# Optimization experiments

Hardware: AMD Instinct MI355X
Metric: run time of the kernel (lower is better)

Reference implementation:

```python
import jax, jax.numpy as jnp
import numpy as np

DIM = 768
HEADS = 12
HIDDEN = 4 * DIM
B, N = 8, 1024
EPS = 1e-5


def setup_inputs() -> dict:
    key = jax.random.key(0)
    ks = jax.random.split(key, 8)
    s = 0.02
    return {
        "x": jax.random.normal(ks[0], (B, N, DIM), dtype=jnp.float32),
        "ln1_g": jnp.ones((DIM,), jnp.float32),
        "ln1_b": jnp.zeros((DIM,), jnp.float32),
        "qkv_w": jax.random.normal(ks[1], (3 * DIM, DIM), jnp.float32) * s,
        "proj_w": jax.random.normal(ks[2], (DIM, DIM), jnp.float32) * s,
        "proj_b": jnp.zeros((DIM,), jnp.float32),
        "ln2_g": jnp.ones((DIM,), jnp.float32),
        "ln2_b": jnp.zeros((DIM,), jnp.float32),
        "fc1_w": jax.random.normal(ks[3], (HIDDEN, DIM), jnp.float32) * s,
        "fc1_b": jnp.zeros((HIDDEN,), jnp.float32),
        "fc2_w": jax.random.normal(ks[4], (DIM, HIDDEN), jnp.float32) * s,
        "fc2_b": jnp.zeros((DIM,), jnp.float32),
    }


def _layernorm(x, g, b):
    mu = jnp.mean(x, axis=-1, keepdims=True)
    var = jnp.mean(jnp.square(x - mu), axis=-1, keepdims=True)
    return (x - mu) * jax.lax.rsqrt(var + EPS) * g + b


def reference(x, ln1_g, ln1_b, qkv_w, proj_w, proj_b, ln2_g, ln2_b, fc1_w, fc1_b, fc2_w, fc2_b):
    Bn, Nn, C = x.shape
    H = HEADS
    D = C // H
    scale = D ** -0.5

    # --- attention branch ---
    h = _layernorm(x, ln1_g, ln1_b)
    qkv = h @ qkv_w.T                      # [B,N,3C] (qkv_bias=False)
    qkv = qkv.reshape(Bn, Nn, 3, H, D)
    q = qkv[:, :, 0].transpose(0, 2, 1, 3)  # [B,H,N,D]
    k = qkv[:, :, 1].transpose(0, 2, 1, 3)
    v = qkv[:, :, 2].transpose(0, 2, 1, 3)
    attn = jnp.einsum('bhnd,bhmd->bhnm', q, k) * scale  # [B,H,N,N]
    attn = jax.nn.softmax(attn, axis=-1)
    ctx = jnp.einsum('bhnm,bhmd->bhnd', attn, v)         # [B,H,N,D]
    ctx = ctx.transpose(0, 2, 1, 3).reshape(Bn, Nn, C)
    x = x + ctx @ proj_w.T + proj_b

    # --- MLP branch ---
    h = _layernorm(x, ln2_g, ln2_b)
    h = jax.nn.gelu(h @ fc1_w.T + fc1_b, approximate=False)
    return x + h @ fc2_w.T + fc2_b
```

## Files before the change

kernel.cpp:

```cpp
#include <hip/hip_runtime.h>
#include <cstdint>

typedef __attribute__((ext_vector_type(8))) short short8;
typedef __attribute__((ext_vector_type(4))) float f32x4;
typedef unsigned short u16t;

__device__ __forceinline__ u16t f2bf(float f) {
  uint32_t u = __float_as_uint(f);
  u += 0x7fffu + ((u >> 16) & 1u);
  return (u16t)(u >> 16);
}

__device__ __forceinline__ uint32_t cvtpk(float lo, float hi) {
  uint32_t r;
  asm("v_cvt_pk_bf16_f32 %0, %1, %2" : "=v"(r) : "v"(lo), "v"(hi));
  return r;
}

__device__ __forceinline__ void gload_lds16(const void* g, void* l) {
  __builtin_amdgcn_global_load_lds(
      (const __attribute__((address_space(1))) void*)g,
      (__attribute__((address_space(3))) void*)l, 16, 0, 0);
}

__global__ __launch_bounds__(256) void cvt_bf16_kernel(const float* __restrict__ in,
                                                       u16t* __restrict__ out, int n8) {
  int i = blockIdx.x * 256 + threadIdx.x;
  if (i >= n8) return;
  const float4* p = (const float4*)in + (size_t)i * 2;
  float4 a = p[0], b = p[1];
  union { short8 v; u16t e[8]; } r;
  r.e[0] = f2bf(a.x); r.e[1] = f2bf(a.y); r.e[2] = f2bf(a.z); r.e[3] = f2bf(a.w);
  r.e[4] = f2bf(b.x); r.e[5] = f2bf(b.y); r.e[6] = f2bf(b.z); r.e[7] = f2bf(b.w);
  *((short8*)out + i) = r.v;
}

__global__ __launch_bounds__(256) void ln_kernel(const float* __restrict__ x,
                                                 const float* __restrict__ g,
                                                 const float* __restrict__ b,
                                                 u16t* __restrict__ out) {
  int row = blockIdx.x, tid = threadIdx.x;
  int wave = tid >> 6, lane = tid & 63;
  const float* xr = x + (size_t)row * 768;
  float v0 = xr[tid], v1 = xr[tid + 256], v2 = xr[tid + 512];
  float s = v0 + v1 + v2;
  float q = v0 * v0 + v1 * v1 + v2 * v2;
#pragma unroll
  for (int m = 32; m >= 1; m >>= 1) {
    s += __shfl_xor(s, m, 64);
    q += __shfl_xor(q, m, 64);
  }
  __shared__ float red[8];
  if (lane == 0) { red[wave] = s; red[4 + wave] = q; }
  __syncthreads();
  s = red[0] + red[1] + red[2] + red[3];
  q = red[4] + red[5] + red[6] + red[7];
  float mu = s * (1.0f / 768.0f);
  float var = q * (1.0f / 768.0f) - mu * mu;
  float rs = rsqrtf(var + 1e-5f);
  u16t* orow = out + (size_t)row * 768;
  orow[tid]       = f2bf((v0 - mu) * rs * g[tid]       + b[tid]);
  orow[tid + 256] = f2bf((v1 - mu) * rs * g[tid + 256] + b[tid + 256]);
  orow[tid + 512] = f2bf((v2 - mu) * rs * g[tid + 512] + b[tid + 512]);
}

template <int EPI, int BM, int MINB>
__global__ __launch_bounds__(256, MINB) void gemm_bt(const u16t* __restrict__ A,
                                                     const u16t* __restrict__ W,
                                                     void* __restrict__ Cout,
                                                     const float* __restrict__ bias,
                                                     const float* __restrict__ res,
                                                     int M, int N, int K) {
  __shared__ __align__(16) u16t As[BM * 64];
  __shared__ __align__(16) u16t Bs[128 * 64];
  constexpr int MF = BM / 32;
  int tid = threadIdx.x;
  int wave = tid >> 6, lane = tid & 63;
  int wr = wave >> 1, wc = wave & 1;
  int bm = blockIdx.y * BM;
  int bn = blockIdx.x * 128;
  f32x4 acc[MF][4] = {};

  int lr = lane >> 3;
  int lc = lane & 7;
  int srcslot = lc ^ lr;
  const u16t* Abase = A + (size_t)(bm + lr) * K + srcslot * 8;
  const u16t* Wbase = W + (size_t)(bn + lr) * K + srcslot * 8;

  for (int kt = 0; kt < K; kt += 64) {
    __syncthreads();
#pragma unroll
    for (int i = 0; i < BM / 32; i++) {
      int chunk = wave * (BM / 32) + i;
      gload_lds16(Abase + (size_t)(chunk * 8) * K + kt, (void*)(As + chunk * 512));
    }
#pragma unroll
    for (int i = 0; i < 4; i++) {
      int chunk = wave * 4 + i;
      gload_lds16(Wbase + (size_t)(chunk * 8) * K + kt, (void*)(Bs + chunk * 512));
    }
    __syncthreads();

    short8 af[MF][2], bfr[4][2];
#pragma unroll
    for (int m = 0; m < MF; m++) {
      int row = wr * (BM / 2) + m * 16 + (lane & 15);
#pragma unroll
      for (int s = 0; s < 2; s++) {
        int slot = s * 4 + (lane >> 4);
        af[m][s] = *(const short8*)(As + row * 64 + ((slot ^ (row & 7)) * 8));
      }
    }
#pragma unroll
    for (int n = 0; n < 4; n++) {
      int row = wc * 64 + n * 16 + (lane & 15);
#pragma unroll
      for (int s = 0; s < 2; s++) {
        int slot = s * 4 + (lane >> 4);
        bfr[n][s] = *(const short8*)(Bs + row * 64 + ((slot ^ (row & 7)) * 8));
      }
    }
    __builtin_amdgcn_s_setprio(1);
#pragma unroll
    for (int m = 0; m < MF; m++)
#pragma unroll
      for (int n = 0; n < 4; n++) {
        acc[m][n] = __builtin_amdgcn_mfma_f32_16x16x32_bf16(af[m][0], bfr[n][0], acc[m][n], 0, 0, 0);
        acc[m][n] = __builtin_amdgcn_mfma_f32_16x16x32_bf16(af[m][1], bfr[n][1], acc[m][n], 0, 0, 0);
      }
    __builtin_amdgcn_s_setprio(0);
  }

#pragma unroll
  for (int m = 0; m < MF; m++) {
#pragma unroll
    for (int n = 0; n < 4; n++) {
      int r0 = bm + wr * (BM / 2) + m * 16 + (lane >> 4) * 4;
      int c = bn + wc * 64 + n * 16 + (lane & 15);
#pragma unroll
      for (int i = 0; i < 4; i++) {
        int r = r0 + i;
        float v = acc[m][n][i];
        if constexpr (EPI == 0) {
          ((u16t*)Cout)[(size_t)r * N + c] = f2bf(v);
        } else if constexpr (EPI == 1) {
          ((float*)Cout)[(size_t)r * N + c] = v + bias[c] + res[(size_t)r * N + c];
        } else {
          v += bias[c];
          float gl = 0.5f * v * (1.0f + erff(v * 0.70710678118f));
          ((u16t*)Cout)[(size_t)r * N + c] = f2bf(gl);
        }
      }
    }
  }
}

__global__ __launch_bounds__(256) void vtrans_kernel(const u16t* __restrict__ qkv,
                                                     u16t* __restrict__ vt) {
  __shared__ u16t T[64][66];
  int h = blockIdx.x % 12, bb = blockIdx.x / 12, kt = blockIdx.y * 64;
  int t = threadIdx.x;
  int r = t >> 2, dc = t & 3;
  const u16t* src = qkv + (size_t)(bb * 1024 + kt + r) * 2304 + 1536 + h * 64 + dc * 16;
  union { uint4 u[2]; u16t e[16]; uint32_t w[8]; } buf;
  buf.u[0] = *(const uint4*)src;
  buf.u[1] = *(const uint4*)(src + 8);
#pragma unroll
  for (int j = 0; j < 8; j++)
    *(uint32_t*)&T[r][dc * 16 + 2 * j] = buf.w[j];
  __syncthreads();
  int d = t >> 2, kc = t & 3;
  union { uint4 u[2]; u16t e[16]; } o;
#pragma unroll
  for (int j = 0; j < 16; j++) o.e[j] = T[kc * 16 + j][d];
  u16t* dst = vt + ((size_t)blockIdx.x * 64 + d) * 1024 + kt + kc * 16;
  *(uint4*)dst = o.u[0];
  *(uint4*)(dst + 8) = o.u[1];
}

__global__ __launch_bounds__(256, 3) void attn_kernel(const u16t* __restrict__ qkv,
                                                      const u16t* __restrict__ vt,
                                                      u16t* __restrict__ ctx) {
  __shared__ __align__(16) u16t Ks[2][64 * 64];
  __shared__ __align__(16) u16t Vs[2][64 * 64];
  __shared__ __align__(16) u16t Plds[4][32 * 72];
  int tid = threadIdx.x;
  int wave = tid >> 6, lane = tid & 63;
  int q = lane & 15, g = lane >> 4;

  int bid = blockIdx.x;
  int xcd = bid & 7, j = bid >> 3;
  int head = xcd + 8 * (j >> 3);
  int qt = (j & 7) * 128 + wave * 32;
  int b = head / 12, h = head % 12;

  const u16t* base = qkv + (size_t)b * 1024 * 2304 + h * 64;
  const u16t* kbase = base + 768;
  const u16t* vtb = vt + (size_t)head * 64 * 1024;

  short8 qf[2][2];
#pragma unroll
  for (int hf = 0; hf < 2; hf++)
#pragma unroll
    for (int hh = 0; hh < 2; hh++)
      qf[hf][hh] = *(const short8*)(base + (size_t)(qt + hf * 16 + q) * 2304 + hh * 32 + g * 8);

  int lr = lane >> 3, lc = lane & 7;
  const u16t* ksrc = kbase + (size_t)lr * 2304 + (size_t)((lc ^ lr) * 8);
  const u16t* vsrc = vtb + (size_t)lr * 1024 + (size_t)((lc ^ lr) * 8);
  int c0 = wave * 2, c1 = wave * 2 + 1;

  auto stage = [&](int kt, int buf) {
    gload_lds16(ksrc + (size_t)(kt + c0 * 8) * 2304, (void*)(Ks[buf] + c0 * 512));
    gload_lds16(ksrc + (size_t)(kt + c1 * 8) * 2304, (void*)(Ks[buf] + c1 * 512));
    gload_lds16(vsrc + (size_t)(c0 * 8) * 1024 + kt, (void*)(Vs[buf] + c0 * 512));
    gload_lds16(vsrc + (size_t)(c1 * 8) * 1024 + kt, (void*)(Vs[buf] + c1 * 512));
  };

  float mA = -1e30f, mB = -1e30f, lA = 0.f, lB = 0.f;
  f32x4 oA[4] = {}, oB[4] = {};
  u16t* Pw = Plds[wave];

  stage(0, 0);
  __syncthreads();

  for (int t = 0; t < 16; ++t) {
    int buf = t & 1;
    if (t < 15) stage((t + 1) * 64, buf ^ 1);

    const u16t* Kb = Ks[buf];
    const u16t* Vb = Vs[buf];

    f32x4 sA[4] = {}, sB[4] = {};
    __builtin_amdgcn_s_setprio(1);
#pragma unroll
    for (int n = 0; n < 4; n++) {
      int row = n * 16 + q;
      short8 k0 = *(const short8*)(Kb + row * 64 + ((g ^ (q & 7)) * 8));
      short8 k1 = *(const short8*)(Kb + row * 64 + (((4 + g) ^ (q & 7)) * 8));
      sA[n] = __builtin_amdgcn_mfma_f32_16x16x32_bf16(k0, qf[0][0], sA[n], 0, 0, 0);
      sA[n] = __builtin_amdgcn_mfma_f32_16x16x32_bf16(k1, qf[0][1], sA[n], 0, 0, 0);
      sB[n] = __builtin_amdgcn_mfma_f32_16x16x32_bf16(k0, qf[1][0], sB[n], 0, 0, 0);
      sB[n] = __builtin_amdgcn_mfma_f32_16x16x32_bf16(k1, qf[1][1], sB[n], 0, 0, 0);
    }
    __builtin_amdgcn_s_setprio(0);

    float alphaA, alphaB;
    {
      float t0 = fmaxf(fmaxf(sA[0][0], sA[0][1]), fmaxf(sA[0][2], sA[0][3]));
      float t1 = fmaxf(fmaxf(sA[1][0], sA[1][1]), fmaxf(sA[1][2], sA[1][3]));
      float t2 = fmaxf(fmaxf(sA[2][0], sA[2][1]), fmaxf(sA[2][2], sA[2][3]));
      float t3 = fmaxf(fmaxf(sA[3][0], sA[3][1]), fmaxf(sA[3][2], sA[3][3]));
      float tm = fmaxf(fmaxf(t0, t1), fmaxf(t2, t3));
      tm = fmaxf(tm, __shfl_xor(tm, 16, 64));
      tm = fmaxf(tm, __shfl_xor(tm, 32, 64));
      float mnew = fmaxf(mA, tm);
      alphaA = __expf((mA - mnew) * 0.125f);
      mA = mnew;
#pragma unroll
      for (int n = 0; n < 4; n++)
#pragma unroll
        for (int i = 0; i < 4; i++) sA[n][i] = __expf((sA[n][i] - mnew) * 0.125f);
      float r0 = (sA[0][0] + sA[0][1]) + (sA[0][2] + sA[0][3]);
      float r1 = (sA[1][0] + sA[1][1]) + (sA[1][2] + sA[1][3]);
      float r2 = (sA[2][0] + sA[2][1]) + (sA[2][2] + sA[2][3]);
      float r3 = (sA[3][0] + sA[3][1]) + (sA[3][2] + sA[3][3]);
      float rs = (r0 + r1) + (r2 + r3);
      rs += __shfl_xor(rs, 16, 64);
      rs += __shfl_xor(rs, 32, 64);
      lA = lA * alphaA + rs;
#pragma unroll
      for (int n = 0; n < 4; n++) {
        uint32_t w0 = cvtpk(sA[n][0], sA[n][1]);
        uint32_t w1 = cvtpk(sA[n][2], sA[n][3]);
        *(uint2*)(Pw + q * 72 + n * 16 + g * 4) = make_uint2(w0, w1);
      }
    }
    {
      float t0 = fmaxf(fmaxf(sB[0][0], sB[0][1]), fmaxf(sB[0][2], sB[0][3]));
      float t1 = fmaxf(fmaxf(sB[1][0], sB[1][1]), fmaxf(sB[1][2], sB[1][3]));
      float t2 = fmaxf(fmaxf(sB[2][0], sB[2][1]), fmaxf(sB[2][2], sB[2][3]));
      float t3 = fmaxf(fmaxf(sB[3][0], sB[3][1]), fmaxf(sB[3][2], sB[3][3]));
      float tm = fmaxf(fmaxf(t0, t1), fmaxf(t2, t3));
      tm = fmaxf(tm, __shfl_xor(tm, 16, 64));
      tm = fmaxf(tm, __shfl_xor(tm, 32, 64));
      float mnew = fmaxf(mB, tm);
      alphaB = __expf((mB - mnew) * 0.125f);
      mB = mnew;
#pragma unroll
      for (int n = 0; n < 4; n++)
#pragma unroll
        for (int i = 0; i < 4; i++) sB[n][i] = __expf((sB[n][i] - mnew) * 0.125f);
      float r0 = (sB[0][0] + sB[0][1]) + (sB[0][2] + sB[0][3]);
      float r1 = (sB[1][0] + sB[1][1]) + (sB[1][2] + sB[1][3]);
      float r2 = (sB[2][0] + sB[2][1]) + (sB[2][2] + sB[2][3]);
      float r3 = (sB[3][0] + sB[3][1]) + (sB[3][2] + sB[3][3]);
      float rs = (r0 + r1) + (r2 + r3);
      rs += __shfl_xor(rs, 16, 64);
      rs += __shfl_xor(rs, 32, 64);
      lB = lB * alphaB + rs;
#pragma unroll
      for (int n = 0; n < 4; n++) {
        uint32_t w0 = cvtpk(sB[n][0], sB[n][1]);
        uint32_t w1 = cvtpk(sB[n][2], sB[n][3]);
        *(uint2*)(Pw + (16 + q) * 72 + n * 16 + g * 4) = make_uint2(w0, w1);
      }
    }

#pragma unroll
    for (int n = 0; n < 4; n++)
#pragma unroll
      for (int i = 0; i < 4; i++) {
        oA[n][i] *= alphaA;
        oB[n][i] *= alphaB;
      }

    short8 pA[2], pB[2];
#pragma unroll
    for (int hh = 0; hh < 2; hh++) {
      pA[hh] = *(const short8*)(Pw + q * 72 + hh * 32 + g * 8);
      pB[hh] = *(const short8*)(Pw + (16 + q) * 72 + hh * 32 + g * 8);
    }
    __builtin_amdgcn_s_setprio(1);
#pragma unroll
    for (int n = 0; n < 4; n++) {
      int row = n * 16 + q;
      short8 v0 = *(const short8*)(Vb + row * 64 + ((g ^ (q & 7)) * 8));
      short8 v1 = *(const short8*)(Vb + row * 64 + (((4 + g) ^ (q & 7)) * 8));
      oA[n] = __builtin_amdgcn_mfma_f32_16x16x32_bf16(v0, pA[0], oA[n], 0, 0, 0);
      oA[n] = __builtin_amdgcn_mfma_f32_16x16x32_bf16(v1, pA[1], oA[n], 0, 0, 0);
      oB[n] = __builtin_amdgcn_mfma_f32_16x16x32_bf16(v0, pB[0], oB[n], 0, 0, 0);
      oB[n] = __builtin_amdgcn_mfma_f32_16x16x32_bf16(v1, pB[1], oB[n], 0, 0, 0);
    }
    __builtin_amdgcn_s_setprio(0);

    __syncthreads();
  }

  float invA = 1.f / lA, invB = 1.f / lB;
  u16t* crowA = ctx + (size_t)(b * 1024 + qt + q) * 768 + h * 64;
  u16t* crowB = ctx + (size_t)(b * 1024 + qt + 16 + q) * 768 + h * 64;
#pragma unroll
  for (int n = 0; n < 4; n++) {
    uint32_t a0 = (uint32_t)f2bf(oA[n][0] * invA) | ((uint32_t)f2bf(oA[n][1] * invA) << 16);
    uint32_t a1 = (uint32_t)f2bf(oA[n][2] * invA) | ((uint32_t)f2bf(oA[n][3] * invA) << 16);
    *(uint32_t*)(crowA + n * 16 + g * 4) = a0;
    *(uint32_t*)(crowA + n * 16 + g * 4 + 2) = a1;
    uint32_t b0 = (uint32_t)f2bf(oB[n][0] * invB) | ((uint32_t)f2bf(oB[n][1] * invB) << 16);
    uint32_t b1 = (uint32_t)f2bf(oB[n][2] * invB) | ((uint32_t)f2bf(oB[n][3] * invB) << 16);
    *(uint32_t*)(crowB + n * 16 + g * 4) = b0;
    *(uint32_t*)(crowB + n * 16 + g * 4 + 2) = b1;
  }
}

extern "C" void kernel_launch(void* const* d_in, const int* in_sizes, int n_in,
                              void* d_out, int out_size, void* d_ws, size_t ws_size,
                              hipStream_t stream) {
  const float* x      = (const float*)d_in[0];
  const float* ln1_g  = (const float*)d_in[1];
  const float* ln1_b  = (const float*)d_in[2];
  const float* qkv_w  = (const float*)d_in[3];
  const float* proj_w = (const float*)d_in[4];
  const float* proj_b = (const float*)d_in[5];
  const float* ln2_g  = (const float*)d_in[6];
  const float* ln2_b  = (const float*)d_in[7];
  const float* fc1_w  = (const float*)d_in[8];
  const float* fc1_b  = (const float*)d_in[9];
  const float* fc2_w  = (const float*)d_in[10];
  const float* fc2_b  = (const float*)d_in[11];

  char* ws = (char*)d_ws;
  u16t* h1   = (u16t*)(ws + 0);
  u16t* qkvb = (u16t*)(ws + 12582912);
  u16t* ctx  = (u16t*)(ws + 50331648);
  float* x2  = (float*)(ws + 62914560);
  u16t* hid  = (u16t*)(ws + 88080384);
  u16t* wq   = (u16t*)(ws + 138412032);
  u16t* wp   = (u16t*)(ws + 141950976);
  u16t* w1   = (u16t*)(ws + 143130624);
  u16t* w2   = (u16t*)(ws + 147849216);
  u16t* vtb  = h1;
  float* out = (float*)d_out;

  cvt_bf16_kernel<<<864, 256, 0, stream>>>(qkv_w, wq, 221184);
  cvt_bf16_kernel<<<288, 256, 0, stream>>>(proj_w, wp, 73728);
  cvt_bf16_kernel<<<1152, 256, 0, stream>>>(fc1_w, w1, 294912);
  cvt_bf16_kernel<<<1152, 256, 0, stream>>>(fc2_w, w2, 294912);

  ln_kernel<<<8192, 256, 0, stream>>>(x, ln1_g, ln1_b, h1);
  gemm_bt<0, 128, 3><<<dim3(18, 64), 256, 0, stream>>>(h1, wq, qkvb, nullptr, nullptr, 8192, 2304, 768);
  vtrans_kernel<<<dim3(96, 16), 256, 0, stream>>>(qkvb, vtb);
  attn_kernel<<<768, 256, 0, stream>>>(qkvb, vtb, ctx);
  gemm_bt<1, 64, 4><<<dim3(6, 128), 256, 0, stream>>>(ctx, wp, x2, proj_b, x, 8192, 768, 768);
  ln_kernel<<<8192, 256, 0, stream>>>(x2, ln2_g, ln2_b, h1);
  gemm_bt<2, 128, 3><<<dim3(24, 64), 256, 0, stream>>>(h1, w1, hid, fc1_b, nullptr, 8192, 3072, 768);
  gemm_bt<1, 64, 4><<<dim3(6, 128), 256, 0, stream>>>(hid, w2, out, fc2_b, x2, 8192, 768, 3072);
}
```

Measured before the change: 265.2 us.

## Replace GEMM with 8-wave double-buffered 128x256 tile kernel and XCD swizzle

Replaces the single-buffered 4-wave GEMM with a 512-thread kernel using 128x256 tiles and LDS double buffering, so the next K-tile loads overlap the MFMA work on the current one. Blocks are remapped with an 8-way interleaved swizzle, and the MFMA operands are swapped so each lane holds 4 consecutive output columns, which allows vectorized packed bf16 and float4 epilogue stores. The larger tiles and one block per CU cut grid sizes a lot (192 blocks for the N=768 GEMMs), which risks under-filling the GPU's CUs and lowering occupancy.

```diff
diff --git a/kernel.cpp b/kernel.cpp
--- a/kernel.cpp
+++ b/kernel.cpp
@@ -64,92 +64,103 @@
   orow[tid + 512] = f2bf((v2 - mu) * rs * g[tid + 512] + b[tid + 512]);
 }
 
-template <int EPI, int BM, int MINB>
-__global__ __launch_bounds__(256, MINB) void gemm_bt(const u16t* __restrict__ A,
-                                                     const u16t* __restrict__ W,
-                                                     void* __restrict__ Cout,
-                                                     const float* __restrict__ bias,
-                                                     const float* __restrict__ res,
-                                                     int M, int N, int K) {
-  __shared__ __align__(16) u16t As[BM * 64];
-  __shared__ __align__(16) u16t Bs[128 * 64];
-  constexpr int MF = BM / 32;
+template <int EPI>
+__global__ __launch_bounds__(512, 1) void gemm8(const u16t* __restrict__ A,
+                                                const u16t* __restrict__ W,
+                                                void* __restrict__ Cout,
+                                                const float* __restrict__ bias,
+                                                const float* __restrict__ res,
+                                                int N, int K, int nbn) {
+  __shared__ __align__(16) u16t As[2][128 * 64];
+  __shared__ __align__(16) u16t Bs[2][256 * 64];
   int tid = threadIdx.x;
-  int wave = tid >> 6, lane = tid & 63;
-  int wr = wave >> 1, wc = wave & 1;
-  int bm = blockIdx.y * BM;
-  int bn = blockIdx.x * 128;
-  f32x4 acc[MF][4] = {};
-
-  int lr = lane >> 3;
-  int lc = lane & 7;
-  int srcslot = lc ^ lr;
-  const u16t* Abase = A + (size_t)(bm + lr) * K + srcslot * 8;
-  const u16t* Wbase = W + (size_t)(bn + lr) * K + srcslot * 8;
-
-  for (int kt = 0; kt < K; kt += 64) {
-    __syncthreads();
-#pragma unroll
-    for (int i = 0; i < BM / 32; i++) {
-      int chunk = wave * (BM / 32) + i;
-      gload_lds16(Abase + (size_t)(chunk * 8) * K + kt, (void*)(As + chunk * 512));
-    }
-#pragma unroll
-    for (int i = 0; i < 4; i++) {
-      int chunk = wave * 4 + i;
-      gload_lds16(Wbase + (size_t)(chunk * 8) * K + kt, (void*)(Bs + chunk * 512));
-    }
-    __syncthreads();
-
-    short8 af[MF][2], bfr[4][2];
-#pragma unroll
-    for (int m = 0; m < MF; m++) {
-      int row = wr * (BM / 2) + m * 16 + (lane & 15);
-#pragma unroll
-      for (int s = 0; s < 2; s++) {
-        int slot = s * 4 + (lane >> 4);
-        af[m][s] = *(const short8*)(As + row * 64 + ((slot ^ (row & 7)) * 8));
+  int wid = tid >> 6, lane = tid & 63;
+  int wr = wid >> 2, wc = wid & 3;
+  int q = lane & 15, g = lane >> 4;
+
+  int nwg = gridDim.x;
+  int bid = blockIdx.x;
+  int swz = (bid & 7) * (nwg >> 3) + (bid >> 3);
+  int bmi = swz / nbn, bni = swz % nbn;
+  int bm = bmi * 128, bn = bni * 256;
+
+  int lr = lane >> 3, lc = lane & 7;
+  const u16t* Asrc = A + (size_t)(bm + lr) * K + ((lc ^ lr) * 8);
+  const u16t* Wsrc = W + (size_t)(bn + lr) * K + ((lc ^ lr) * 8);
+
+  int gi = wid & 3;
+  int ca0 = wr * 8 + gi * 2;
+  int hB = wc >> 1;
+  int gj = (wid & 1) | ((wid >> 2) << 1);
+  int cb0 = hB * 16 + gj * 4;
+
+  f32x4 acc[4][4] = {};
+
+  auto stage = [&](int kt, int db) {
+    gload_lds16(Asrc + (size_t)(ca0 * 8) * K + kt, (void*)(As[db] + ca0 * 512));
+    gload_lds16(Asrc + (size_t)(ca0 * 8 + 8) * K + kt, (void*)(As[db] + ca0 * 512 + 512));
+#pragma unroll
+    for (int j = 0; j < 4; j++)
+      gload_lds16(Wsrc + (size_t)((cb0 + j) * 8) * K + kt, (void*)(Bs[db] + (cb0 + j) * 512));
+  };
+
+  stage(0, 0);
+  __syncthreads();
+
+  int NT = K >> 6;
+  for (int T = 0; T < NT; ++T) {
+    int db = T & 1;
+    if (T + 1 < NT) stage((T + 1) * 64, db ^ 1);
+    const u16t* Ab = As[db];
+    const u16t* Bb = Bs[db];
+#pragma unroll
+    for (int kh = 0; kh < 2; kh++) {
+      short8 af[4], bf[4];
+#pragma unroll
+      for (int x = 0; x < 4; x++) {
+        int slot = ((kh * 4 + g) ^ (q & 7)) * 8;
+        af[x] = *(const short8*)(Ab + (wr * 64 + x * 16 + q) * 64 + slot);
+        bf[x] = *(const short8*)(Bb + (wc * 64 + x * 16 + q) * 64 + slot);
       }
-    }
-#pragma unroll
-    for (int n = 0; n < 4; n++) {
-      int row = wc * 64 + n * 16 + (lane & 15);
-#pragma unroll
-      for (int s = 0; s < 2; s++) {
-        int slot = s * 4 + (lane >> 4);
-        bfr[n][s] = *(const short8*)(Bs + row * 64 + ((slot ^ (row & 7)) * 8));
-      }
-    }
-    __builtin_amdgcn_s_setprio(1);
-#pragma unroll
-    for (int m = 0; m < MF; m++)
-#pragma unroll
-      for (int n = 0; n < 4; n++) {
-        acc[m][n] = __builtin_amdgcn_mfma_f32_16x16x32_bf16(af[m][0], bfr[n][0], acc[m][n], 0, 0, 0);
-        acc[m][n] = __builtin_amdgcn_mfma_f32_16x16x32_bf16(af[m][1], bfr[n][1], acc[m][n], 0, 0, 0);
-      }
-    __builtin_amdgcn_s_setprio(0);
+      __builtin_amdgcn_s_barrier();
+      __builtin_amdgcn_s_setprio(1);
+#pragma unroll
+      for (int mf = 0; mf < 4; mf++)
+#pragma unroll
+        for (int nf = 0; nf < 4; nf++)
+          acc[mf][nf] = __builtin_amdgcn_mfma_f32_16x16x32_bf16(bf[nf], af[mf], acc[mf][nf], 0, 0, 0);
+      __builtin_amdgcn_s_setprio(0);
+      if (kh == 1) asm volatile("s_waitcnt vmcnt(0)" ::: "memory");
+      __builtin_amdgcn_s_barrier();
+    }
   }
 
 #pragma unroll
-  for (int m = 0; m < MF; m++) {
-#pragma unroll
-    for (int n = 0; n < 4; n++) {
-      int r0 = bm + wr * (BM / 2) + m * 16 + (lane >> 4) * 4;
-      int c = bn + wc * 64 + n * 16 + (lane & 15);
-#pragma unroll
-      for (int i = 0; i < 4; i++) {
-        int r = r0 + i;
-        float v = acc[m][n][i];
-        if constexpr (EPI == 0) {
-          ((u16t*)Cout)[(size_t)r * N + c] = f2bf(v);
-        } else if constexpr (EPI == 1) {
-          ((float*)Cout)[(size_t)r * N + c] = v + bias[c] + res[(size_t)r * N + c];
-        } else {
-          v += bias[c];
-          float gl = 0.5f * v * (1.0f + erff(v * 0.70710678118f));
-          ((u16t*)Cout)[(size_t)r * N + c] = f2bf(gl);
-        }
+  for (int mf = 0; mf < 4; mf++) {
+    int m = bm + wr * 64 + mf * 16 + q;
+#pragma unroll
+    for (int nf = 0; nf < 4; nf++) {
+      int n = bn + wc * 64 + nf * 16 + g * 4;
+      f32x4 v = acc[mf][nf];
+      if constexpr (EPI == 0) {
+        uint2 pk = make_uint2(cvtpk(v[0], v[1]), cvtpk(v[2], v[3]));
+        *(uint2*)((u16t*)Cout + (size_t)m * N + n) = pk;
+      } else if constexpr (EPI == 1) {
+        const float4 bv = *(const float4*)(bias + n);
+        const float4 rv = *(const float4*)(res + (size_t)m * N + n);
+        float4 o;
+        o.x = v[0] + bv.x + rv.x; o.y = v[1] + bv.y + rv.y;
+        o.z = v[2] + bv.z + rv.z; o.w = v[3] + bv.w + rv.w;
+        *(float4*)((float*)Cout + (size_t)m * N + n) = o;
+      } else {
+        const float4 bv = *(const float4*)(bias + n);
+        float t0 = v[0] + bv.x, t1 = v[1] + bv.y, t2 = v[2] + bv.z, t3 = v[3] + bv.w;
+        t0 = 0.5f * t0 * (1.0f + erff(t0 * 0.70710678118f));
+        t1 = 0.5f * t1 * (1.0f + erff(t1 * 0.70710678118f));
+        t2 = 0.5f * t2 * (1.0f + erff(t2 * 0.70710678118f));
+        t3 = 0.5f * t3 * (1.0f + erff(t3 * 0.70710678118f));
+        uint2 pk = make_uint2(cvtpk(t0, t1), cvtpk(t2, t3));
+        *(uint2*)((u16t*)Cout + (size_t)m * N + n) = pk;
       }
     }
   }
@@ -388,11 +399,11 @@
   cvt_bf16_kernel<<<1152, 256, 0, stream>>>(fc2_w, w2, 294912);
 
   ln_kernel<<<8192, 256, 0, stream>>>(x, ln1_g, ln1_b, h1);
-  gemm_bt<0, 128, 3><<<dim3(18, 64), 256, 0, stream>>>(h1, wq, qkvb, nullptr, nullptr, 8192, 2304, 768);
+  gemm8<0><<<576, 512, 0, stream>>>(h1, wq, qkvb, nullptr, nullptr, 2304, 768, 9);
   vtrans_kernel<<<dim3(96, 16), 256, 0, stream>>>(qkvb, vtb);
   attn_kernel<<<768, 256, 0, stream>>>(qkvb, vtb, ctx);
-  gemm_bt<1, 64, 4><<<dim3(6, 128), 256, 0, stream>>>(ctx, wp, x2, proj_b, x, 8192, 768, 768);
+  gemm8<1><<<192, 512, 0, stream>>>(ctx, wp, x2, proj_b, x, 768, 768, 3);
   ln_kernel<<<8192, 256, 0, stream>>>(x2, ln2_g, ln2_b, h1);
-  gemm_bt<2, 128, 3><<<dim3(24, 64), 256, 0, stream>>>(h1, w1, hid, fc1_b, nullptr, 8192, 3072, 768);
-  gemm_bt<1, 64, 4><<<dim3(6, 128), 256, 0, stream>>>(hid, w2, out, fc2_b, x2, 8192, 768, 3072);
-}
+  gemm8<2><<<768, 512, 0, stream>>>(h1, w1, hid, fc1_b, nullptr, 3072, 768, 12);
+  gemm8<1><<<192, 512, 0, stream>>>(hid, w2, out, fc2_b, x2, 768, 3072, 3);
+}
```

New measurement: 315.2 us. 18.8% more time.

## Double-buffer GEMM LDS tiles and vectorize epilogue via swapped MFMA operands

Applied to the files above, without the earlier changes.

The GEMM now keeps two LDS buffers and issues the global-to-LDS loads for the next K tile before computing on the current one, which drops one barrier per iteration and overlaps memory with MFMA work. Swapping the MFMA A/B operands transposes the accumulator layout, so each lane holds four consecutive columns and the epilogue can use packed bf16 and float4 stores and loads instead of scalar ones. LDS use doubles, so the min-blocks-per-CU hints are lowered, which may reduce occupancy.

```diff
diff --git a/kernel.cpp b/kernel.cpp
--- a/kernel.cpp
+++ b/kernel.cpp
@@ -71,85 +71,97 @@
                                                      const float* __restrict__ bias,
                                                      const float* __restrict__ res,
                                                      int M, int N, int K) {
-  __shared__ __align__(16) u16t As[BM * 64];
-  __shared__ __align__(16) u16t Bs[128 * 64];
+  __shared__ __align__(16) u16t As[2][BM * 64];
+  __shared__ __align__(16) u16t Bs[2][128 * 64];
   constexpr int MF = BM / 32;
   int tid = threadIdx.x;
   int wave = tid >> 6, lane = tid & 63;
   int wr = wave >> 1, wc = wave & 1;
+  int q = lane & 15, g = lane >> 4;
   int bm = blockIdx.y * BM;
   int bn = blockIdx.x * 128;
   f32x4 acc[MF][4] = {};
 
-  int lr = lane >> 3;
-  int lc = lane & 7;
-  int srcslot = lc ^ lr;
-  const u16t* Abase = A + (size_t)(bm + lr) * K + srcslot * 8;
-  const u16t* Wbase = W + (size_t)(bn + lr) * K + srcslot * 8;
-
-  for (int kt = 0; kt < K; kt += 64) {
-    __syncthreads();
+  int lr = lane >> 3, lc = lane & 7;
+  const u16t* Abase = A + (size_t)(bm + lr) * K + ((lc ^ lr) * 8);
+  const u16t* Wbase = W + (size_t)(bn + lr) * K + ((lc ^ lr) * 8);
+
+  auto stage = [&](int kt, int db) {
 #pragma unroll
     for (int i = 0; i < BM / 32; i++) {
       int chunk = wave * (BM / 32) + i;
-      gload_lds16(Abase + (size_t)(chunk * 8) * K + kt, (void*)(As + chunk * 512));
+      gload_lds16(Abase + (size_t)(chunk * 8) * K + kt, (void*)(As[db] + chunk * 512));
     }
 #pragma unroll
     for (int i = 0; i < 4; i++) {
       int chunk = wave * 4 + i;
-      gload_lds16(Wbase + (size_t)(chunk * 8) * K + kt, (void*)(Bs + chunk * 512));
-    }
-    __syncthreads();
+      gload_lds16(Wbase + (size_t)(chunk * 8) * K + kt, (void*)(Bs[db] + chunk * 512));
+    }
+  };
+
+  stage(0, 0);
+  __syncthreads();
+
+  int NT = K >> 6;
+  for (int t = 0; t < NT; ++t) {
+    int db = t & 1;
+    if (t + 1 < NT) stage((t + 1) * 64, db ^ 1);
+    const u16t* Ab = As[db];
+    const u16t* Bb = Bs[db];
 
     short8 af[MF][2], bfr[4][2];
 #pragma unroll
     for (int m = 0; m < MF; m++) {
-      int row = wr * (BM / 2) + m * 16 + (lane & 15);
-#pragma unroll
-      for (int s = 0; s < 2; s++) {
-        int slot = s * 4 + (lane >> 4);
-        af[m][s] = *(const short8*)(As + row * 64 + ((slot ^ (row & 7)) * 8));
-      }
+      int row = wr * (BM / 2) + m * 16 + q;
+#pragma unroll
+      for (int s = 0; s < 2; s++)
+        af[m][s] = *(const short8*)(Ab + row * 64 + (((s * 4 + g) ^ (row & 7)) * 8));
     }
 #pragma unroll
     for (int n = 0; n < 4; n++) {
-      int row = wc * 64 + n * 16 + (lane & 15);
-#pragma unroll
-      for (int s = 0; s < 2; s++) {
-        int slot = s * 4 + (lane >> 4);
-        bfr[n][s] = *(const short8*)(Bs + row * 64 + ((slot ^ (row & 7)) * 8));
-      }
+      int row = wc * 64 + n * 16 + q;
+#pragma unroll
+      for (int s = 0; s < 2; s++)
+        bfr[n][s] = *(const short8*)(Bb + row * 64 + (((s * 4 + g) ^ (row & 7)) * 8));
     }
     __builtin_amdgcn_s_setprio(1);
 #pragma unroll
     for (int m = 0; m < MF; m++)
 #pragma unroll
       for (int n = 0; n < 4; n++) {
-        acc[m][n] = __builtin_amdgcn_mfma_f32_16x16x32_bf16(af[m][0], bfr[n][0], acc[m][n], 0, 0, 0);
-        acc[m][n] = __builtin_amdgcn_mfma_f32_16x16x32_bf16(af[m][1], bfr[n][1], acc[m][n], 0, 0, 0);
+        acc[m][n] = __builtin_amdgcn_mfma_f32_16x16x32_bf16(bfr[n][0], af[m][0], acc[m][n], 0, 0, 0);
+        acc[m][n] = __builtin_amdgcn_mfma_f32_16x16x32_bf16(bfr[n][1], af[m][1], acc[m][n], 0, 0, 0);
       }
     __builtin_amdgcn_s_setprio(0);
+    __syncthreads();
   }
 
 #pragma unroll
   for (int m = 0; m < MF; m++) {
+    int r = bm + wr * (BM / 2) + m * 16 + q;
 #pragma unroll
     for (int n = 0; n < 4; n++) {
-      int r0 = bm + wr * (BM / 2) + m * 16 + (lane >> 4) * 4;
-      int c = bn + wc * 64 + n * 16 + (lane & 15);
-#pragma unroll
-      for (int i = 0; i < 4; i++) {
-        int r = r0 + i;
-        float v = acc[m][n][i];
-        if constexpr (EPI == 0) {
-          ((u16t*)Cout)[(size_t)r * N + c] = f2bf(v);
-        } else if constexpr (EPI == 1) {
-          ((float*)Cout)[(size_t)r * N + c] = v + bias[c] + res[(size_t)r * N + c];
-        } else {
-          v += bias[c];
-          float gl = 0.5f * v * (1.0f + erff(v * 0.70710678118f));
-          ((u16t*)Cout)[(size_t)r * N + c] = f2bf(gl);
-        }
+      int c = bn + wc * 64 + n * 16 + g * 4;
+      f32x4 v = acc[m][n];
+      if constexpr (EPI == 0) {
+        uint2 pk = make_uint2(cvtpk(v[0], v[1]), cvtpk(v[2], v[3]));
+        *(uint2*)((u16t*)Cout + (size_t)r * N + c) = pk;
+      } else if constexpr (EPI == 1) {
+        const float4 bv = *(const float4*)(bias + c);
+        const float4 rv = *(const float4*)(res + (size_t)r * N + c);
+        float4 o;
+        o.x = v[0] + bv.x + rv.x; o.y = v[1] + bv.y + rv.y;
+        o.z = v[2] + bv.z + rv.z; o.w = v[3] + bv.w + rv.w;
+        *(float4*)((float*)Cout + (size_t)r * N + c) = o;
+      } else {
+        const float4 bv = *(const float4*)(bias + c);
+        float t0 = v[0] + bv.x, t1 = v[1] + bv.y, t2 = v[2] + bv.z, t3 = v[3] + bv.w;
+        t0 = 0.5f * t0 * (1.0f + erff(t0 * 0.70710678118f));
+        t1 = 0.5f * t1 * (1.0f + erff(t1 * 0.70710678118f));
+        t2 = 0.5f * t2 * (1.0f + erff(t2 * 0.70710678118f));
+        t3 = 0.5f * t3 * (1.0f + erff(t3 * 0.70710678118f));
+        uint2 pk = make_uint2(cvtpk(t0, t1), cvtpk(t2, t3));
+        *(uint2*)((u16t*)Cout + (size_t)r * N + c) = pk;
       }
     }
   }
@@ -388,11 +400,11 @@
   cvt_bf16_kernel<<<1152, 256, 0, stream>>>(fc2_w, w2, 294912);
 
   ln_kernel<<<8192, 256, 0, stream>>>(x, ln1_g, ln1_b, h1);
-  gemm_bt<0, 128, 3><<<dim3(18, 64), 256, 0, stream>>>(h1, wq, qkvb, nullptr, nullptr, 8192, 2304, 768);
+  gemm_bt<0, 128, 2><<<dim3(18, 64), 256, 0, stream>>>(h1, wq, qkvb, nullptr, nullptr, 8192, 2304, 768);
   vtrans_kernel<<<dim3(96, 16), 256, 0, stream>>>(qkvb, vtb);
   attn_kernel<<<768, 256, 0, stream>>>(qkvb, vtb, ctx);
-  gemm_bt<1, 64, 4><<<dim3(6, 128), 256, 0, stream>>>(ctx, wp, x2, proj_b, x, 8192, 768, 768);
+  gemm_bt<1, 64, 3><<<dim3(6, 128), 256, 0, stream>>>(ctx, wp, x2, proj_b, x, 8192, 768, 768);
   ln_kernel<<<8192, 256, 0, stream>>>(x2, ln2_g, ln2_b, h1);
-  gemm_bt<2, 128, 3><<<dim3(24, 64), 256, 0, stream>>>(h1, w1, hid, fc1_b, nullptr, 8192, 3072, 768);
-  gemm_bt<1, 64, 4><<<dim3(6, 128), 256, 0, stream>>>(hid, w2, out, fc2_b, x2, 8192, 768, 3072);
-}
+  gemm_bt<2, 128, 2><<<dim3(24, 64), 256, 0, stream>>>(h1, w1, hid, fc1_b, nullptr, 8192, 3072, 768);
+  gemm_bt<1, 64, 3><<<dim3(6, 128), 256, 0, stream>>>(hid, w2, out, fc2_b, x2, 8192, 768, 3072);
+}
```

New measurement: 287.4 us. 1.08x slower.
